# Performance work log

Measured on AMD Instinct MI355X. Metric: run time of the kernel, lower is better.

## Reference

```python
import jax, jax.numpy as jnp
import numpy as np

DIM = 512
HEADS = 8
HEAD_DIM = DIM // HEADS


def setup_inputs() -> dict:
    key = jax.random.key(0)
    ks = jax.random.split(key, 8)
    B, T, C, H, W = 2, 8, DIM, 16, 16
    s = lambda fan: 1.0 / np.sqrt(fan)
    return {
        "features_seq": jax.random.normal(ks[0], (B, T, C, H, W), jnp.float32),
        # weights stored as [in, out] (math identical to torch Linear y = x @ W.T)
        "qkv_w": jax.random.normal(ks[1], (C, 3 * C), jnp.float32) * s(C),
        "qkv_b": jnp.zeros((3 * C,), jnp.float32),
        "proj_w": jax.random.normal(ks[2], (C, C), jnp.float32) * s(C),
        "proj_b": jnp.zeros((C,), jnp.float32),
        "ln1_g": jnp.ones((C,), jnp.float32),
        "ln1_b": jnp.zeros((C,), jnp.float32),
        "w1": jax.random.normal(ks[3], (C, 4 * C), jnp.float32) * s(C),
        "b1": jnp.zeros((4 * C,), jnp.float32),
        "w2": jax.random.normal(ks[4], (4 * C, C), jnp.float32) * s(4 * C),
        "b2": jnp.zeros((C,), jnp.float32),
        "ln2_g": jnp.ones((C,), jnp.float32),
        "ln2_b": jnp.zeros((C,), jnp.float32),
    }


def _layernorm(x, g, b, eps=1e-5):
    mu = jnp.mean(x, axis=-1, keepdims=True)
    var = jnp.var(x, axis=-1, keepdims=True)
    return (x - mu) * jax.lax.rsqrt(var + eps) * g + b


def _mhsa(x, qkv_w, qkv_b, proj_w, proj_b):
    B, N, C = x.shape
    qkv = (x @ qkv_w + qkv_b).reshape(B, N, 3, HEADS, HEAD_DIM)
    qkv = jnp.transpose(qkv, (2, 0, 3, 1, 4))  # [3, B, h, N, d]
    q, k, v = qkv[0], qkv[1], qkv[2]
    scale = HEAD_DIM ** -0.5
    attn = jnp.einsum("bhqd,bhkd->bhqk", q, k) * scale
    attn = jax.nn.softmax(attn, axis=-1)
    o = jnp.einsum("bhqk,bhkd->bhqd", attn, v)
    o = jnp.transpose(o, (0, 2, 1, 3)).reshape(B, N, C)
    return o @ proj_w + proj_b


def reference(features_seq, qkv_w, qkv_b, proj_w, proj_b, ln1_g, ln1_b,
              w1, b1, w2, b2, ln2_g, ln2_b):
    B, T, C, H, W = features_seq.shape
    L = H * W
    # [B,T,C,H,W] -> [B, T*L, C]
    x = features_seq.reshape(B, T, C, L).transpose(0, 1, 3, 2).reshape(B, T * L, C)
    x = x + _mhsa(_layernorm(x, ln1_g, ln1_b), qkv_w, qkv_b, proj_w, proj_b)
    h = _layernorm(x, ln2_g, ln2_b)
    h = jax.nn.gelu(h @ w1 + b1, approximate=False) @ w2 + b2
    x = x + h
    # back to [B, T, C, H, W]
    out = x.reshape(B, T, L, C).transpose(0, 1, 3, 2).reshape(B, T, C, H, W)
    return out
```

## Files before the change

kernel.cpp:

```cpp
#include <hip/hip_runtime.h>
#include <stdint.h>
#include <math.h>

typedef __attribute__((ext_vector_type(8))) short short8;
typedef __attribute__((ext_vector_type(4))) float f32x4;
typedef __attribute__((ext_vector_type(4))) ushort ushort4v;

__device__ __forceinline__ ushort f2bf(float f) {
    union { float f; uint32_t i; } v; v.f = f;
    uint32_t r = v.i + 0x7FFFu + ((v.i >> 16) & 1u);
    return (ushort)(r >> 16);
}
__device__ __forceinline__ float bf2f(ushort u) {
    union { uint32_t i; float f; } v; v.i = ((uint32_t)u) << 16; return v.f;
}

__device__ __forceinline__ void gload_lds16(const ushort* gp, ushort* lp) {
    __builtin_amdgcn_global_load_lds(
        (const __attribute__((address_space(1))) void*)gp,
        (__attribute__((address_space(3))) void*)lp, 16, 0, 0);
}

__global__ __launch_bounds__(512) void prep_kernel(const float* __restrict__ in,
        const float* __restrict__ g, const float* __restrict__ bta,
        float* __restrict__ x, ushort* __restrict__ xln) {
    int token = blockIdx.x;
    int c = threadIdx.x;
    int b = token >> 11;
    int n = token & 2047;
    int t = n >> 8;
    int l = n & 255;
    size_t iidx = (((size_t)((b * 8 + t) * 512 + c)) << 8) + l;
    float v = in[iidx];
    x[(size_t)token * 512 + c] = v;

    float s = v, s2 = v * v;
    #pragma unroll
    for (int off = 32; off > 0; off >>= 1) {
        s  += __shfl_down(s, off, 64);
        s2 += __shfl_down(s2, off, 64);
    }
    __shared__ float ps[8], ps2[8];
    int wave = threadIdx.x >> 6, lane = threadIdx.x & 63;
    if (lane == 0) { ps[wave] = s; ps2[wave] = s2; }
    __syncthreads();
    float mu = 0.f, m2 = 0.f;
    #pragma unroll
    for (int i = 0; i < 8; i++) { mu += ps[i]; m2 += ps2[i]; }
    mu *= (1.0f / 512.0f); m2 *= (1.0f / 512.0f);
    float rs = rsqrtf(m2 - mu * mu + 1e-5f);
    float y = (v - mu) * rs * g[c] + bta[c];
    xln[(size_t)token * 512 + c] = f2bf(y);
}

__global__ __launch_bounds__(512) void ln2_kernel(const float* __restrict__ xin,
        const float* __restrict__ g, const float* __restrict__ bta,
        ushort* __restrict__ out) {
    int token = blockIdx.x;
    int c = threadIdx.x;
    float v = xin[(size_t)token * 512 + c];
    float s = v, s2 = v * v;
    #pragma unroll
    for (int off = 32; off > 0; off >>= 1) {
        s  += __shfl_down(s, off, 64);
        s2 += __shfl_down(s2, off, 64);
    }
    __shared__ float ps[8], ps2[8];
    int wave = threadIdx.x >> 6, lane = threadIdx.x & 63;
    if (lane == 0) { ps[wave] = s; ps2[wave] = s2; }
    __syncthreads();
    float mu = 0.f, m2 = 0.f;
    #pragma unroll
    for (int i = 0; i < 8; i++) { mu += ps[i]; m2 += ps2[i]; }
    mu *= (1.0f / 512.0f); m2 *= (1.0f / 512.0f);
    float rs = rsqrtf(m2 - mu * mu + 1e-5f);
    float y = (v - mu) * rs * g[c] + bta[c];
    out[(size_t)token * 512 + c] = f2bf(y);
}

__global__ __launch_bounds__(256) void wtrans_kernel(
        const float* __restrict__ wa, ushort* __restrict__ ta,
        const float* __restrict__ wb, ushort* __restrict__ tb,
        const float* __restrict__ wc, ushort* __restrict__ tc,
        const float* __restrict__ wd, ushort* __restrict__ td) {
    __shared__ float tile[32][33];
    int bid = blockIdx.x;
    const float* W; ushort* T; int K, N, tn, tk;
    if (bid < 768)       { W = wa; T = ta; K = 512;  N = 1536; tn = bid % 48; tk = bid / 48; }
    else if (bid < 1024) { bid -= 768;  W = wb; T = tb; K = 512;  N = 512;  tn = bid % 16; tk = bid / 16; }
    else if (bid < 2048) { bid -= 1024; W = wc; T = tc; K = 512;  N = 2048; tn = bid % 64; tk = bid / 64; }
    else                 { bid -= 2048; W = wd; T = td; K = 2048; N = 512;  tn = bid % 16; tk = bid / 16; }
    int n0 = tn * 32, k0 = tk * 32;
    int tx = threadIdx.x & 31, ty = threadIdx.x >> 5;
    #pragma unroll
    for (int i = 0; i < 4; i++)
        tile[ty + i * 8][tx] = W[(size_t)(k0 + ty + i * 8) * N + n0 + tx];
    __syncthreads();
    #pragma unroll
    for (int i = 0; i < 4; i++) {
        int nn = ty + i * 8;
        T[(size_t)(n0 + nn) * K + k0 + tx] = f2bf(tile[tx][nn]);
    }
}

#define EPI_BF16    0
#define EPI_F32RES  1
#define EPI_GELU    2
#define EPI_F32PART 3

template<int EPI>
__global__ __launch_bounds__(256) void gemm_kernel(
        const ushort* __restrict__ A, const ushort* __restrict__ Bt,
        const float* __restrict__ bias, const float* __restrict__ resid,
        float* __restrict__ outF, float* __restrict__ outF2,
        ushort* __restrict__ outB, int M, int N, int K) {
    __shared__ __align__(16) ushort As[64 * 64];
    __shared__ __align__(16) ushort Bs[128 * 64];
    int tid = threadIdx.x;
    int wave = tid >> 6, lane = tid & 63;
    int l16 = lane & 15, quad = lane >> 4;
    int wc = wave;
    int m0 = blockIdx.y * 64, n0 = blockIdx.x * 128;
    int Ksp = K / gridDim.z;
    int kbeg = blockIdx.z * Ksp, kend = kbeg + Ksp;

    f32x4 acc[4][2] = {};
    for (int k0 = kbeg; k0 < kend; k0 += 64) {
        #pragma unroll
        for (int c = 0; c < 2; c++) {
            int slot = c * 256 + tid;
            int row = slot >> 3, ch = slot & 7;
            gload_lds16(A + (size_t)(m0 + row) * K + k0 + ch * 8,
                        As + (size_t)(c * 256 + wave * 64) * 8);
        }
        #pragma unroll
        for (int c = 0; c < 4; c++) {
            int slot = c * 256 + tid;
            int row = slot >> 3, ch = slot & 7;
            gload_lds16(Bt + (size_t)(n0 + row) * K + k0 + ch * 8,
                        Bs + (size_t)(c * 256 + wave * 64) * 8);
        }
        __syncthreads();
        #pragma unroll
        for (int kk = 0; kk < 2; kk++) {
            short8 af[4], bf[2];
            #pragma unroll
            for (int i = 0; i < 4; i++)
                af[i] = *(const short8*)&As[(i * 16 + l16) * 64 + kk * 32 + quad * 8];
            #pragma unroll
            for (int j = 0; j < 2; j++)
                bf[j] = *(const short8*)&Bs[(wc * 32 + j * 16 + l16) * 64 + kk * 32 + quad * 8];
            #pragma unroll
            for (int i = 0; i < 4; i++)
                #pragma unroll
                for (int j = 0; j < 2; j++)
                    acc[i][j] = __builtin_amdgcn_mfma_f32_16x16x32_bf16(af[i], bf[j], acc[i][j], 0, 0, 0);
        }
        __syncthreads();
    }
    float* oP = (EPI == EPI_F32PART && blockIdx.z == 1) ? outF2 : outF;
    #pragma unroll
    for (int i = 0; i < 4; i++) {
        int row_base = m0 + i * 16 + quad * 4;
        #pragma unroll
        for (int j = 0; j < 2; j++) {
            int col = n0 + wc * 32 + j * 16 + l16;
            float bvf = (EPI == EPI_F32PART) ? 0.f : bias[col];
            #pragma unroll
            for (int r = 0; r < 4; r++) {
                int row = row_base + r;
                float v = acc[i][j][r] + bvf;
                if constexpr (EPI == EPI_F32RES) {
                    outF[(size_t)row * N + col] = v + resid[(size_t)row * N + col];
                } else if constexpr (EPI == EPI_F32PART) {
                    oP[(size_t)row * N + col] = v;
                } else if constexpr (EPI == EPI_GELU) {
                    float gg = 0.5f * v * (1.0f + erff(v * 0.70710678118654752f));
                    outB[(size_t)row * N + col] = f2bf(gg);
                } else {
                    outB[(size_t)row * N + col] = f2bf(v);
                }
            }
        }
    }
}

__global__ __launch_bounds__(512) void flash_kernel(const ushort* __restrict__ qkv,
        ushort* __restrict__ o) {
    __shared__ __align__(16) char smem[47232];
    auto Ks  = (ushort (*)[64][72])smem;
    auto Vt  = (ushort (*)[4640])(smem + 18432);
    auto Pt  = (ushort (*)[16][40])(smem + 36992);
    auto cbuf = (float (*)[18][64])smem;

    int tid = threadIdx.x;
    int wave = tid >> 6, lane = tid & 63;
    int kh = wave >> 2;
    int wq = wave & 3;
    int l16 = lane & 15, quad = lane >> 4;
    int bidx = blockIdx.x;
    int qt = bidx & 31;
    int h = (bidx >> 5) & 7;
    int b = bidx >> 8;
    int q0 = qt * 64;
    const size_t base = (size_t)b * 2048 * 1536;

    int htid = tid & 255;
    int srow = htid >> 2;
    int sg   = htid & 3;
    int sdb  = sg * 16;
    const ushort* kgbase = qkv + base + 512  + h * 64 + sdb;
    const ushort* vgbase = qkv + base + 1024 + h * 64 + sdb;
    int vldsoff = sdb * 72 + sg * 8 + srow;

    short8 aq[2];
    {
        int qrow = q0 + wq * 16 + l16;
        const ushort* qp = qkv + base + (size_t)qrow * 1536 + h * 64;
        aq[0] = *(const short8*)(qp + quad * 8);
        aq[1] = *(const short8*)(qp + 32 + quad * 8);
    }
    f32x4 accO[4] = {};
    float mrow = -INFINITY, lrow = 0.f;

    {
        int kb = kh * 1024;
        const ushort* kp = kgbase + (size_t)(kb + srow) * 1536;
        short8 k0 = *(const short8*)kp;
        short8 k1 = *(const short8*)(kp + 8);
        const ushort* vp = vgbase + (size_t)(kb + srow) * 1536;
        short8 v0 = *(const short8*)vp;
        short8 v1 = *(const short8*)(vp + 8);
        *(short8*)&Ks[kh][srow][sdb]     = k0;
        *(short8*)&Ks[kh][srow][sdb + 8] = k1;
        #pragma unroll
        for (int i = 0; i < 8; i++) Vt[kh][vldsoff + i * 72] = (ushort)v0[i];
        #pragma unroll
        for (int i = 0; i < 8; i++) Vt[kh][vldsoff + (8 + i) * 72] = (ushort)v1[i];
    }
    __syncthreads();

    for (int it = 0; it < 16; ++it) {
        short8 nk0, nk1, nv0, nv1;
        bool pre = (it < 15);
        if (pre) {
            int kb = kh * 1024 + (it + 1) * 64;
            const ushort* kp = kgbase + (size_t)(kb + srow) * 1536;
            nk0 = *(const short8*)kp;
            nk1 = *(const short8*)(kp + 8);
            const ushort* vp = vgbase + (size_t)(kb + srow) * 1536;
            nv0 = *(const short8*)vp;
            nv1 = *(const short8*)(vp + 8);
        }
        f32x4 sacc[4] = {};
        __builtin_amdgcn_s_setprio(1);
        #pragma unroll
        for (int c = 0; c < 2; c++) {
            #pragma unroll
            for (int s = 0; s < 4; s++) {
                short8 kf = *(short8*)&Ks[kh][s * 16 + l16][c * 32 + quad * 8];
                sacc[s] = __builtin_amdgcn_mfma_f32_16x16x32_bf16(kf, aq[c], sacc[s], 0, 0, 0);
            }
        }
        __builtin_amdgcn_s_setprio(0);
        float tm = sacc[0][0];
        #pragma unroll
        for (int s = 0; s < 4; s++)
            #pragma unroll
            for (int r = 0; r < 4; r++) tm = fmaxf(tm, sacc[s][r]);
        tm = fmaxf(tm, __shfl_xor(tm, 16, 64));
        tm = fmaxf(tm, __shfl_xor(tm, 32, 64));
        float mn = fmaxf(mrow, tm * 0.125f);
        float al = __expf(mrow - mn);
        float rsum = 0.f;
        ushort4v w4[4];
        #pragma unroll
        for (int s = 0; s < 4; s++)
            #pragma unroll
            for (int r = 0; r < 4; r++) {
                float pv = __expf(sacc[s][r] * 0.125f - mn);
                rsum += pv;
                w4[s][r] = f2bf(pv);
            }
        rsum += __shfl_xor(rsum, 16, 64);
        rsum += __shfl_xor(rsum, 32, 64);
        lrow = lrow * al + rsum;
        mrow = mn;
        #pragma unroll
        for (int s = 0; s < 4; s++)
            #pragma unroll
            for (int r = 0; r < 4; r++) accO[s][r] *= al;
        *(ushort4v*)&Pt[wave][l16][quad * 4]      = w4[0];
        *(ushort4v*)&Pt[wave][l16][16 + quad * 4] = w4[1];
        {
            short8 ap = *(short8*)&Pt[wave][l16][quad * 8];
            __builtin_amdgcn_s_setprio(1);
            #pragma unroll
            for (int s = 0; s < 4; s++) {
                short8 vf = *(short8*)&Vt[kh][(s * 16 + l16) * 72 + s * 8 + quad * 8];
                accO[s] = __builtin_amdgcn_mfma_f32_16x16x32_bf16(vf, ap, accO[s], 0, 0, 0);
            }
            __builtin_amdgcn_s_setprio(0);
        }
        *(ushort4v*)&Pt[wave][l16][quad * 4]      = w4[2];
        *(ushort4v*)&Pt[wave][l16][16 + quad * 4] = w4[3];
        {
            short8 ap = *(short8*)&Pt[wave][l16][quad * 8];
            __builtin_amdgcn_s_setprio(1);
            #pragma unroll
            for (int s = 0; s < 4; s++) {
                short8 vf = *(short8*)&Vt[kh][(s * 16 + l16) * 72 + s * 8 + 32 + quad * 8];
                accO[s] = __builtin_amdgcn_mfma_f32_16x16x32_bf16(vf, ap, accO[s], 0, 0, 0);
            }
            __builtin_amdgcn_s_setprio(0);
        }
        __syncthreads();
        if (pre) {
            *(short8*)&Ks[kh][srow][sdb]     = nk0;
            *(short8*)&Ks[kh][srow][sdb + 8] = nk1;
            #pragma unroll
            for (int i = 0; i < 8; i++) Vt[kh][vldsoff + i * 72] = (ushort)nv0[i];
            #pragma unroll
            for (int i = 0; i < 8; i++) Vt[kh][vldsoff + (8 + i) * 72] = (ushort)nv1[i];
        }
        __syncthreads();
    }
    if (kh == 1) {
        cbuf[wq][0][lane] = mrow;
        cbuf[wq][1][lane] = lrow;
        #pragma unroll
        for (int s = 0; s < 4; s++)
            #pragma unroll
            for (int r = 0; r < 4; r++)
                cbuf[wq][2 + s * 4 + r][lane] = accO[s][r];
    }
    __syncthreads();
    if (kh == 0) {
        float m1 = cbuf[wq][0][lane];
        float l1 = cbuf[wq][1][lane];
        float mn = fmaxf(mrow, m1);
        float a0 = __expf(mrow - mn);
        float a1 = __expf(m1 - mn);
        float rl = 1.0f / (lrow * a0 + l1 * a1);
        int qrow = q0 + wq * 16 + l16;
        #pragma unroll
        for (int s = 0; s < 4; s++) {
            ushort4v ov4;
            #pragma unroll
            for (int r = 0; r < 4; r++) {
                float ov = (accO[s][r] * a0 + cbuf[wq][2 + s * 4 + r][lane] * a1) * rl;
                ov4[r] = f2bf(ov);
            }
            *(ushort4v*)&o[((size_t)(b * 2048 + qrow)) * 512 + h * 64 + s * 16 + quad * 4] = ov4;
        }
    }
}

__global__ __launch_bounds__(256) void tout_kernel(const float* __restrict__ x2,
        const float* __restrict__ pA, const float* __restrict__ pB,
        const float* __restrict__ b2, float* __restrict__ out) {
    __shared__ float tile[32][33];
    int bt = blockIdx.z;
    int l0 = blockIdx.y * 32;
    int c0 = blockIdx.x * 32;
    int tx = threadIdx.x, ty = threadIdx.y;
    float bv = b2[c0 + tx];
    #pragma unroll
    for (int i = 0; i < 4; i++) {
        int l = ty + i * 8;
        size_t idx = ((size_t)bt * 256 + l0 + l) * 512 + c0 + tx;
        tile[l][tx] = x2[idx] + pA[idx] + pB[idx] + bv;
    }
    __syncthreads();
    #pragma unroll
    for (int i = 0; i < 4; i++) {
        int cc = ty + i * 8;
        out[((size_t)bt * 512 + c0 + cc) * 256 + l0 + tx] = tile[tx][cc];
    }
}

extern "C" void kernel_launch(void* const* d_in, const int* in_sizes, int n_in,
                              void* d_out, int out_size, void* d_ws, size_t ws_size,
                              hipStream_t stream) {
    const float* in_feat = (const float*)d_in[0];
    const float* qkv_w  = (const float*)d_in[1];
    const float* qkv_b  = (const float*)d_in[2];
    const float* proj_w = (const float*)d_in[3];
    const float* proj_b = (const float*)d_in[4];
    const float* ln1_g  = (const float*)d_in[5];
    const float* ln1_b  = (const float*)d_in[6];
    const float* w1     = (const float*)d_in[7];
    const float* b1     = (const float*)d_in[8];
    const float* w2     = (const float*)d_in[9];
    const float* b2     = (const float*)d_in[10];
    const float* ln2_g  = (const float*)d_in[11];
    const float* ln2_b  = (const float*)d_in[12];

    char* ws = (char*)d_ws;
    float*  x    = (float*) (ws);
    float*  x2   = (float*) (ws + 8388608);
    ushort* xln  = (ushort*)(ws + 16777216);
    ushort* h2   = (ushort*)(ws + 20971520);
    ushort* ao   = (ushort*)(ws + 25165824);
    ushort* qkv  = (ushort*)(ws + 29360128);
    ushort* gbuf = (ushort*)(ws + 41943040);

    float* pA = (float*)(ws);
    float* pB = (float*)(ws + 16777216);

    char* scr = (char*)d_out;
    ushort* qkvT = (ushort*)(scr);
    ushort* projT = (ushort*)(scr + 1572864);
    ushort* w1T  = (ushort*)(scr + 2097152);
    ushort* w2T  = (ushort*)(scr + 4194304);

    wtrans_kernel<<<3072, 256, 0, stream>>>(qkv_w, qkvT, proj_w, projT,
                                            w1, w1T, w2, w2T);
    prep_kernel<<<4096, 512, 0, stream>>>(in_feat, ln1_g, ln1_b, x, xln);
    gemm_kernel<EPI_BF16><<<dim3(12, 64), 256, 0, stream>>>(
        xln, qkvT, qkv_b, nullptr, nullptr, nullptr, qkv, 4096, 1536, 512);
    flash_kernel<<<512, 512, 0, stream>>>(qkv, ao);
    gemm_kernel<EPI_F32RES><<<dim3(4, 64), 256, 0, stream>>>(
        ao, projT, proj_b, x, x2, nullptr, nullptr, 4096, 512, 512);
    ln2_kernel<<<4096, 512, 0, stream>>>(x2, ln2_g, ln2_b, h2);
    gemm_kernel<EPI_GELU><<<dim3(16, 64), 256, 0, stream>>>(
        h2, w1T, b1, nullptr, nullptr, nullptr, gbuf, 4096, 2048, 512);
    gemm_kernel<EPI_F32PART><<<dim3(4, 64, 2), 256, 0, stream>>>(
        gbuf, w2T, nullptr, nullptr, pA, pB, nullptr, 4096, 512, 2048);
    tout_kernel<<<dim3(16, 8, 16), dim3(32, 8), 0, stream>>>(
        x2, pA, pB, b2, (float*)d_out);
}
```

Measured before the change: 230.3 us.

## Double-buffer GEMM LDS tiles and use 128-row tiles for QKV and FC1

The GEMM kernel now keeps two LDS buffers and issues the global-to-LDS loads for the next K tile before computing on the current one, so load latency can overlap the MFMA work. A BM template parameter selects 128-row tiles (2x2 wave layout, four N fragments per wave) for the QKV and FC1 GEMMs, halving their grid and increasing operand reuse per block. The cost is more LDS per block (up to 64 KB) and more accumulator registers, which may reduce occupancy. There is only one barrier per iteration, so LDS reuse relies on that barrier ordering the prefetch against the previous reads.

```diff
diff --git a/kernel.cpp b/kernel.cpp
--- a/kernel.cpp
+++ b/kernel.cpp
@@ -108,52 +108,63 @@
 #define EPI_GELU    2
 #define EPI_F32PART 3
 
-template<int EPI>
+template<int EPI, int BM>
 __global__ __launch_bounds__(256) void gemm_kernel(
         const ushort* __restrict__ A, const ushort* __restrict__ Bt,
         const float* __restrict__ bias, const float* __restrict__ resid,
         float* __restrict__ outF, float* __restrict__ outF2,
         ushort* __restrict__ outB, int M, int N, int K) {
-    __shared__ __align__(16) ushort As[64 * 64];
-    __shared__ __align__(16) ushort Bs[128 * 64];
+    __shared__ __align__(16) ushort As[2][BM * 64];
+    __shared__ __align__(16) ushort Bs[2][128 * 64];
     int tid = threadIdx.x;
     int wave = tid >> 6, lane = tid & 63;
     int l16 = lane & 15, quad = lane >> 4;
-    int wc = wave;
-    int m0 = blockIdx.y * 64, n0 = blockIdx.x * 128;
+    constexpr int NJ = (BM == 128) ? 4 : 2;
+    constexpr int WCW = (BM == 128) ? 64 : 32;
+    int wr = (BM == 128) ? (wave >> 1) : 0;
+    int wc = (BM == 128) ? (wave & 1) : wave;
+    int m0 = blockIdx.y * BM, n0 = blockIdx.x * 128;
     int Ksp = K / gridDim.z;
-    int kbeg = blockIdx.z * Ksp, kend = kbeg + Ksp;
-
-    f32x4 acc[4][2] = {};
-    for (int k0 = kbeg; k0 < kend; k0 += 64) {
-        #pragma unroll
-        for (int c = 0; c < 2; c++) {
+    int kbeg = blockIdx.z * Ksp;
+
+    auto stage = [&](int bi, int k0) {
+        #pragma unroll
+        for (int c = 0; c < BM / 32; c++) {
             int slot = c * 256 + tid;
             int row = slot >> 3, ch = slot & 7;
             gload_lds16(A + (size_t)(m0 + row) * K + k0 + ch * 8,
-                        As + (size_t)(c * 256 + wave * 64) * 8);
+                        &As[bi][(c * 256 + wave * 64) * 8]);
         }
         #pragma unroll
         for (int c = 0; c < 4; c++) {
             int slot = c * 256 + tid;
             int row = slot >> 3, ch = slot & 7;
             gload_lds16(Bt + (size_t)(n0 + row) * K + k0 + ch * 8,
-                        Bs + (size_t)(c * 256 + wave * 64) * 8);
-        }
-        __syncthreads();
+                        &Bs[bi][(c * 256 + wave * 64) * 8]);
+        }
+    };
+
+    f32x4 acc[4][NJ] = {};
+    int nt = Ksp >> 6;
+    stage(0, kbeg);
+    __syncthreads();
+    for (int t = 0; t < nt; ++t) {
+        int cur = t & 1;
+        if (t + 1 < nt) stage(cur ^ 1, kbeg + ((t + 1) << 6));
+        __builtin_amdgcn_sched_barrier(0);
         #pragma unroll
         for (int kk = 0; kk < 2; kk++) {
-            short8 af[4], bf[2];
+            short8 af[4], bf[NJ];
             #pragma unroll
             for (int i = 0; i < 4; i++)
-                af[i] = *(const short8*)&As[(i * 16 + l16) * 64 + kk * 32 + quad * 8];
-            #pragma unroll
-            for (int j = 0; j < 2; j++)
-                bf[j] = *(const short8*)&Bs[(wc * 32 + j * 16 + l16) * 64 + kk * 32 + quad * 8];
+                af[i] = *(const short8*)&As[cur][(wr * 64 + i * 16 + l16) * 64 + kk * 32 + quad * 8];
+            #pragma unroll
+            for (int j = 0; j < NJ; j++)
+                bf[j] = *(const short8*)&Bs[cur][(wc * WCW + j * 16 + l16) * 64 + kk * 32 + quad * 8];
             #pragma unroll
             for (int i = 0; i < 4; i++)
                 #pragma unroll
-                for (int j = 0; j < 2; j++)
+                for (int j = 0; j < NJ; j++)
                     acc[i][j] = __builtin_amdgcn_mfma_f32_16x16x32_bf16(af[i], bf[j], acc[i][j], 0, 0, 0);
         }
         __syncthreads();
@@ -161,10 +172,10 @@
     float* oP = (EPI == EPI_F32PART && blockIdx.z == 1) ? outF2 : outF;
     #pragma unroll
     for (int i = 0; i < 4; i++) {
-        int row_base = m0 + i * 16 + quad * 4;
-        #pragma unroll
-        for (int j = 0; j < 2; j++) {
-            int col = n0 + wc * 32 + j * 16 + l16;
+        int row_base = m0 + wr * 64 + i * 16 + quad * 4;
+        #pragma unroll
+        for (int j = 0; j < NJ; j++) {
+            int col = n0 + wc * WCW + j * 16 + l16;
             float bvf = (EPI == EPI_F32PART) ? 0.f : bias[col];
             #pragma unroll
             for (int r = 0; r < 4; r++) {
@@ -417,15 +428,15 @@
     wtrans_kernel<<<3072, 256, 0, stream>>>(qkv_w, qkvT, proj_w, projT,
                                             w1, w1T, w2, w2T);
     prep_kernel<<<4096, 512, 0, stream>>>(in_feat, ln1_g, ln1_b, x, xln);
-    gemm_kernel<EPI_BF16><<<dim3(12, 64), 256, 0, stream>>>(
+    gemm_kernel<EPI_BF16, 128><<<dim3(12, 32), 256, 0, stream>>>(
         xln, qkvT, qkv_b, nullptr, nullptr, nullptr, qkv, 4096, 1536, 512);
     flash_kernel<<<512, 512, 0, stream>>>(qkv, ao);
-    gemm_kernel<EPI_F32RES><<<dim3(4, 64), 256, 0, stream>>>(
+    gemm_kernel<EPI_F32RES, 64><<<dim3(4, 64), 256, 0, stream>>>(
         ao, projT, proj_b, x, x2, nullptr, nullptr, 4096, 512, 512);
     ln2_kernel<<<4096, 512, 0, stream>>>(x2, ln2_g, ln2_b, h2);
-    gemm_kernel<EPI_GELU><<<dim3(16, 64), 256, 0, stream>>>(
+    gemm_kernel<EPI_GELU, 128><<<dim3(16, 32), 256, 0, stream>>>(
         h2, w1T, b1, nullptr, nullptr, nullptr, gbuf, 4096, 2048, 512);
-    gemm_kernel<EPI_F32PART><<<dim3(4, 64, 2), 256, 0, stream>>>(
+    gemm_kernel<EPI_F32PART, 64><<<dim3(4, 64, 2), 256, 0, stream>>>(
         gbuf, w2T, nullptr, nullptr, pA, pB, nullptr, 4096, 512, 2048);
     tout_kernel<<<dim3(16, 8, 16), dim3(32, 8), 0, stream>>>(
         x2, pA, pB, b2, (float*)d_out);
```

Result: no change. 233.3 us (+1.3%).

## Double-buffer GEMM tiles via register prefetch with padded LDS and swizzled block order

Applied to the files above, without the earlier changes.

Replaces the direct global-to-LDS loads with register-staged prefetching two K-tiles ahead into double-buffered shared memory. This lets global loads overlap MFMA compute and drops one barrier per iteration. It also pads LDS rows to 72 elements to reduce bank conflicts, and remaps block indices to group tiles for better L2 locality. In exchange it uses more registers and LDS, which may lower occupancy.

```diff
diff --git a/kernel.cpp b/kernel.cpp
--- a/kernel.cpp
+++ b/kernel.cpp
@@ -13,12 +13,6 @@
 }
 __device__ __forceinline__ float bf2f(ushort u) {
     union { uint32_t i; float f; } v; v.i = ((uint32_t)u) << 16; return v.f;
-}
-
-__device__ __forceinline__ void gload_lds16(const ushort* gp, ushort* lp) {
-    __builtin_amdgcn_global_load_lds(
-        (const __attribute__((address_space(1))) void*)gp,
-        (__attribute__((address_space(3))) void*)lp, 16, 0, 0);
 }
 
 __global__ __launch_bounds__(512) void prep_kernel(const float* __restrict__ in,
@@ -108,55 +102,101 @@
 #define EPI_GELU    2
 #define EPI_F32PART 3
 
+#define GISSUE(S, KT) do { \
+    pa##S##0 = *(const short8*)(agp0 + (KT)); \
+    pa##S##1 = *(const short8*)(agp1 + (KT)); \
+    pb##S##0 = *(const short8*)(bgp0 + (KT)); \
+    pb##S##1 = *(const short8*)(bgp1 + (KT)); \
+    pb##S##2 = *(const short8*)(bgp2 + (KT)); \
+    pb##S##3 = *(const short8*)(bgp3 + (KT)); \
+} while (0)
+
+#define GWRITE(BUF, S) do { \
+    *(short8*)&As[BUF][aw0] = pa##S##0; \
+    *(short8*)&As[BUF][aw1] = pa##S##1; \
+    *(short8*)&Bs[BUF][bw0] = pb##S##0; \
+    *(short8*)&Bs[BUF][bw1] = pb##S##1; \
+    *(short8*)&Bs[BUF][bw2] = pb##S##2; \
+    *(short8*)&Bs[BUF][bw3] = pb##S##3; \
+} while (0)
+
+#define GCOMPUTE(BUF) do { \
+    _Pragma("unroll") \
+    for (int kk = 0; kk < 2; kk++) { \
+        short8 af[4], bf[2]; \
+        _Pragma("unroll") \
+        for (int i = 0; i < 4; i++) \
+            af[i] = *(const short8*)&As[BUF][(i * 16 + l16) * 72 + kk * 32 + quad * 8]; \
+        _Pragma("unroll") \
+        for (int j = 0; j < 2; j++) \
+            bf[j] = *(const short8*)&Bs[BUF][(wc * 32 + j * 16 + l16) * 72 + kk * 32 + quad * 8]; \
+        _Pragma("unroll") \
+        for (int i = 0; i < 4; i++) \
+            _Pragma("unroll") \
+            for (int j = 0; j < 2; j++) \
+                acc[i][j] = __builtin_amdgcn_mfma_f32_16x16x32_bf16(af[i], bf[j], acc[i][j], 0, 0, 0); \
+    } \
+} while (0)
+
+#define GSYNC() do { \
+    asm volatile("s_waitcnt lgkmcnt(0)" ::: "memory"); \
+    __builtin_amdgcn_sched_barrier(0); \
+    __builtin_amdgcn_s_barrier(); \
+    __builtin_amdgcn_sched_barrier(0); \
+} while (0)
+
 template<int EPI>
 __global__ __launch_bounds__(256) void gemm_kernel(
         const ushort* __restrict__ A, const ushort* __restrict__ Bt,
         const float* __restrict__ bias, const float* __restrict__ resid,
         float* __restrict__ outF, float* __restrict__ outF2,
         ushort* __restrict__ outB, int M, int N, int K) {
-    __shared__ __align__(16) ushort As[64 * 64];
-    __shared__ __align__(16) ushort Bs[128 * 64];
+    __shared__ __align__(16) ushort As[2][64 * 72];
+    __shared__ __align__(16) ushort Bs[2][128 * 72];
     int tid = threadIdx.x;
     int wave = tid >> 6, lane = tid & 63;
     int l16 = lane & 15, quad = lane >> 4;
     int wc = wave;
-    int m0 = blockIdx.y * 64, n0 = blockIdx.x * 128;
+    int gx = gridDim.x, gy = gridDim.y;
+    int p = blockIdx.y * gx + blockIdx.x;
+    int cpx = (gx * gy) >> 3;
+    int L = (p & 7) * cpx + (p >> 3);
+    int bx = L / gy, by = L % gy;
+    int m0 = by * 64, n0 = bx * 128;
     int Ksp = K / gridDim.z;
-    int kbeg = blockIdx.z * Ksp, kend = kbeg + Ksp;
-
+    int kbeg = blockIdx.z * Ksp;
+    int nt = Ksp >> 6;
+
+    int trow = tid >> 3, ch = tid & 7;
+    const ushort* agp0 = A  + (size_t)(m0 + trow) * K + kbeg + ch * 8;
+    const ushort* agp1 = A  + (size_t)(m0 + 32 + trow) * K + kbeg + ch * 8;
+    const ushort* bgp0 = Bt + (size_t)(n0 + trow) * K + kbeg + ch * 8;
+    const ushort* bgp1 = Bt + (size_t)(n0 + 32 + trow) * K + kbeg + ch * 8;
+    const ushort* bgp2 = Bt + (size_t)(n0 + 64 + trow) * K + kbeg + ch * 8;
+    const ushort* bgp3 = Bt + (size_t)(n0 + 96 + trow) * K + kbeg + ch * 8;
+    int aw0 = trow * 72 + ch * 8, aw1 = (32 + trow) * 72 + ch * 8;
+    int bw0 = trow * 72 + ch * 8, bw1 = (32 + trow) * 72 + ch * 8;
+    int bw2 = (64 + trow) * 72 + ch * 8, bw3 = (96 + trow) * 72 + ch * 8;
+
+    short8 pa00, pa01, pb00, pb01, pb02, pb03;
+    short8 pa10, pa11, pb10, pb11, pb12, pb13;
     f32x4 acc[4][2] = {};
-    for (int k0 = kbeg; k0 < kend; k0 += 64) {
-        #pragma unroll
-        for (int c = 0; c < 2; c++) {
-            int slot = c * 256 + tid;
-            int row = slot >> 3, ch = slot & 7;
-            gload_lds16(A + (size_t)(m0 + row) * K + k0 + ch * 8,
-                        As + (size_t)(c * 256 + wave * 64) * 8);
-        }
-        #pragma unroll
-        for (int c = 0; c < 4; c++) {
-            int slot = c * 256 + tid;
-            int row = slot >> 3, ch = slot & 7;
-            gload_lds16(Bt + (size_t)(n0 + row) * K + k0 + ch * 8,
-                        Bs + (size_t)(c * 256 + wave * 64) * 8);
-        }
-        __syncthreads();
-        #pragma unroll
-        for (int kk = 0; kk < 2; kk++) {
-            short8 af[4], bf[2];
-            #pragma unroll
-            for (int i = 0; i < 4; i++)
-                af[i] = *(const short8*)&As[(i * 16 + l16) * 64 + kk * 32 + quad * 8];
-            #pragma unroll
-            for (int j = 0; j < 2; j++)
-                bf[j] = *(const short8*)&Bs[(wc * 32 + j * 16 + l16) * 64 + kk * 32 + quad * 8];
-            #pragma unroll
-            for (int i = 0; i < 4; i++)
-                #pragma unroll
-                for (int j = 0; j < 2; j++)
-                    acc[i][j] = __builtin_amdgcn_mfma_f32_16x16x32_bf16(af[i], bf[j], acc[i][j], 0, 0, 0);
-        }
-        __syncthreads();
+
+    GISSUE(0, 0);
+    GISSUE(1, 64);
+    GWRITE(0, 0);
+    GSYNC();
+    for (int t = 0; t < nt; t += 2) {
+        if (t + 2 < nt) GISSUE(0, (t + 2) << 6);
+        __builtin_amdgcn_sched_barrier(0);
+        GCOMPUTE(0);
+        if (t + 1 < nt) GWRITE(1, 1);
+        GSYNC();
+        if (t + 3 < nt) GISSUE(1, (t + 3) << 6);
+        __builtin_amdgcn_sched_barrier(0);
+        if (t + 1 < nt) GCOMPUTE(1);
+        if (t + 2 < nt) GWRITE(0, 0);
+        GSYNC();
     }
     float* oP = (EPI == EPI_F32PART && blockIdx.z == 1) ? outF2 : outF;
     #pragma unroll
```

Measured after the change: 228.9 us. About the same (-0.6%).
